# Kernel optimization log

Hardware: AMD Instinct MI355X
Metric: run time of the kernel (lower is better)

The kernel has to match this reference:

```python
import jax, jax.numpy as jnp
import numpy as np

N, E, H, NF, MN, ME = 4096, 65536, 128, 4, 8, 4
DEPTH, RATIO, NT = 5, 0.2, 2


def _k_list():
    ks, n = [], N
    for _ in range(DEPTH):
        n = int(np.ceil(RATIO * n))
        ks.append(n)
    return ks

K_LIST = _k_list()  # [820, 164, 33, 7, 2]


def _gcn(A, x, W, b, fill):
    # GCNConv on dense adjacency: D^-1/2 (A + fill*I) D^-1/2 @ (x W) + b
    n = A.shape[0]
    Ah = A + fill * jnp.eye(n, dtype=A.dtype)
    deg = jnp.sum(Ah, axis=1)
    dinv = jnp.where(deg > 0, jax.lax.rsqrt(jnp.maximum(deg, 1e-12)), 0.0)
    return (dinv[:, None] * Ah * dinv[None, :]) @ (x @ W) + b


def _augment(A):
    # GraphUNet.augment_adj: remove self loops, add weight-1 loops, A@A, remove self loops
    n = A.shape[0]
    eye = jnp.eye(n, dtype=A.dtype)
    A1 = A * (1.0 - eye) + eye
    A2 = A1 @ A1
    return A2 * (1.0 - eye)


def _topk_pool(A, x, w, k):
    # TopKPooling: score = tanh(x.w / ||w||), keep top-k, scale kept features by score
    score = jnp.tanh((x @ w) / jnp.linalg.norm(w))
    sv, perm = jax.lax.top_k(score, k)
    return x[perm] * sv[:, None], A[perm][:, perm], perm


def _graph_unet(A0, x, Wd0, bd0, Wd, bd, pool_w, Wu, bu):
    act = jax.nn.relu
    x = act(_gcn(A0, x, Wd0, bd0, 2.0))  # improved GCN: fill=2
    xs, As, perms = [x], [A0], []
    A = A0
    for i in range(DEPTH):
        A = _augment(A)
        x, A, perm = _topk_pool(A, x, pool_w[i], K_LIST[i])
        x = act(_gcn(A, x, Wd[i], bd[i], 2.0))
        if i < DEPTH - 1:
            xs.append(x)
            As.append(A)
        perms.append(perm)
    for i in range(DEPTH):
        j = DEPTH - 1 - i
        res, Aj, perm = xs[j], As[j], perms[j]
        up = jnp.zeros_like(res).at[perm].set(x)
        x = _gcn(Aj, res + up, Wu[i], bu[i], 2.0)  # sum_res=True
        if i < DEPTH - 1:
            x = act(x)
    return x


def _forward(F_0, mesh_node, mesh_edge, Wm, bm, Wd0, bd0, Wd, bd, pool_w,
             Wu, bu, Wout, bout, edge_index, n_time):
    src, dst = edge_index[0], edge_index[1]
    A = jnp.zeros((N, N), jnp.float32).at[dst, src].add(1.0)  # dst aggregates from src
    h = jnp.zeros((N, H), jnp.float32)
    F_cur = F_0
    Fs = []
    for _ in range(n_time):
        node_attr = jnp.concatenate([F_cur, mesh_node, h], axis=1)
        # Input: per-edge cat([x_i, x_j, e]) -> Linear -> scatter-sum by dst
        msg = jnp.concatenate([node_attr[dst], node_attr[src], mesh_edge], axis=1) @ Wm + bm
        h1 = jax.nn.relu(jax.ops.segment_sum(msg, dst, num_segments=N))
        h2 = _graph_unet(A, h1, Wd0, bd0, Wd, bd, pool_w, Wu, bu)
        h = jax.lax.stop_gradient(h2)
        h2 = jax.nn.relu(h2)
        F_next = _gcn(A, jnp.concatenate([h1, h2], axis=1), Wout, bout, 1.0)
        Fs.append(F_next)
        F_cur = jax.lax.stop_gradient(F_next)
    return jnp.stack(Fs, axis=1)  # [N, n_time, NF]


def setup_inputs() -> dict:
    key = jax.random.key(0)
    ks = jax.random.split(key, 12)
    s = 0.05
    node_in = NF + MN + H
    return {
        "F_0": jax.random.normal(ks[0], (N, NF), jnp.float32),
        "mesh_node": jax.random.normal(ks[1], (N, MN), jnp.float32),
        "mesh_edge": jax.random.normal(ks[2], (E, ME), jnp.float32),
        "Wm": jax.random.normal(ks[3], (2 * node_in + ME, H), jnp.float32) * s,
        "bm": jnp.zeros((H,), jnp.float32),
        "Wd0": jax.random.normal(ks[4], (H, H), jnp.float32) * s,
        "bd0": jnp.zeros((H,), jnp.float32),
        "Wd": jax.random.normal(ks[5], (DEPTH, H, H), jnp.float32) * s,
        "bd": jnp.zeros((DEPTH, H), jnp.float32),
        "pool_w": jax.random.normal(ks[6], (DEPTH, H), jnp.float32) * s,
        "Wu": jax.random.normal(ks[7], (DEPTH, H, H), jnp.float32) * s,
        "bu": jnp.zeros((DEPTH, H), jnp.float32),
        "Wout": jax.random.normal(ks[8], (2 * H, NF), jnp.float32) * s,
        "bout": jnp.zeros((NF,), jnp.float32),
        "edge_index": jax.random.randint(ks[9], (2, E), 0, N, dtype=jnp.int32),
        "n_time": NT,
    }


def reference(F_0, mesh_node, mesh_edge, Wm, bm, Wd0, bd0, Wd, bd, pool_w,
              Wu, bu, Wout, bout, edge_index, n_time):
    return _forward(F_0, mesh_node, mesh_edge, Wm, bm, Wd0, bd0, Wd, bd,
                    pool_w, Wu, bu, Wout, bout, edge_index, n_time)
```

## Files before the change

kernel.cpp:

```cpp
#include <hip/hip_runtime.h>
#include <math.h>

#define NN 4096
#define EE 65536
#define H 128
#define NF 4
#define MNODE 8
#define MEDGE 4
#define NT 2

__global__ void k_count(const int* __restrict__ dst, int* __restrict__ cnt) {
  int e = blockIdx.x * 256 + threadIdx.x;
  if (e < EE) atomicAdd(&cnt[dst[e]], 1);
}

__global__ void k_scan(const int* __restrict__ cnt, int* __restrict__ rp) {
  __shared__ int sh[1024];
  int t = threadIdx.x;
  int v0 = cnt[4*t], v1 = cnt[4*t+1], v2 = cnt[4*t+2], v3 = cnt[4*t+3];
  int p1 = v0, p2 = v0 + v1, p3 = p2 + v2, tot = p3 + v3;
  sh[t] = tot; __syncthreads();
  for (int off = 1; off < 1024; off <<= 1) {
    int add = (t >= off) ? sh[t-off] : 0;
    __syncthreads();
    sh[t] += add;
    __syncthreads();
  }
  int base = sh[t] - tot;
  rp[4*t] = base; rp[4*t+1] = base + p1; rp[4*t+2] = base + p2; rp[4*t+3] = base + p3;
  if (t == 1023) rp[NN] = sh[t];
}

__global__ void k_fill(const int* __restrict__ ei, int* __restrict__ cursor, int* __restrict__ cols) {
  int e = blockIdx.x * 256 + threadIdx.x;
  if (e < EE) {
    int d = ei[EE + e], s = ei[e];
    int pos = atomicAdd(&cursor[d], 1);
    cols[pos] = s;
  }
}

__global__ void k_dinv0(const int* __restrict__ cnt, float* __restrict__ d2, float* __restrict__ d1) {
  int i = blockIdx.x * 256 + threadIdx.x;
  if (i < NN) {
    float c = (float)cnt[i];
    d2[i] = 1.f / sqrtf(c + 2.f);
    d1[i] = 1.f / sqrtf(c + 1.f);
  }
}

__global__ void k_pwnorm(const float* __restrict__ pw, float* __restrict__ pwn) {
  int l = blockIdx.x, t = threadIdx.x;
  float a = pw[l*H + t], b = pw[l*H + 64 + t];
  float s = a*a + b*b;
  for (int off = 32; off > 0; off >>= 1) s += __shfl_down(s, off);
  if (t == 0) pwn[l] = sqrtf(s);
}

__global__ void k_segS(const int* __restrict__ dst, const float* __restrict__ me, float* __restrict__ S) {
  int e = blockIdx.x * 256 + threadIdx.x;
  if (e < EE) {
    int d = dst[e];
#pragma unroll
    for (int m = 0; m < MEDGE; m++) atomicAdd(&S[d*MEDGE + m], me[e*MEDGE + m]);
  }
}

__device__ __forceinline__ void score_epilogue(float v, int row, int t,
                                               const float* pw, const float* pwn1,
                                               float* scoreo, unsigned long long* keyso,
                                               int* ranko, float* r2) {
  float sp = v * pw[t];
  for (int off = 32; off > 0; off >>= 1) sp += __shfl_down(sp, off);
  if ((t & 63) == 0) r2[t >> 6] = sp;
  __syncthreads();
  if (t == 0) {
    float s = r2[0] + r2[1];
    float sc = tanhf(s / pwn1[0]);
    scoreo[row] = sc;
    float s2 = sc + 0.0f;
    unsigned u = __float_as_uint(s2);
    u ^= (unsigned)(((int)u >> 31)) | 0x80000000u;
    keyso[row] = ((unsigned long long)u << 12) | (unsigned)(4095 - row);
    ranko[row] = 0;
  }
}

__global__ void k_mm_cat(const float* __restrict__ F, const float* __restrict__ mn,
                         const float* __restrict__ h, const float* __restrict__ Wm,
                         float* __restrict__ P, float* __restrict__ Q) {
  __shared__ float as[140];
  int row = blockIdx.x, t = threadIdx.x;
  for (int c = t; c < 140; c += 128) {
    float v;
    if (c < NF) v = F[row*NF + c];
    else if (c < NF + MNODE) v = mn[row*MNODE + (c - NF)];
    else v = h[(size_t)row*H + (c - NF - MNODE)];
    as[c] = v;
  }
  __syncthreads();
  const float* BQ = Wm + 140*H;
  float ap = 0.f, aq = 0.f;
  for (int kk = 0; kk < 140; kk++) {
    float a = as[kk];
    ap += a * Wm[kk*H + t];
    aq += a * BQ[kk*H + t];
  }
  P[(size_t)row*H + t] = ap;
  Q[(size_t)row*H + t] = aq;
}

__global__ void k_spmm_h1_mm(const float* __restrict__ Q, const int* __restrict__ rp,
                             const int* __restrict__ cols, const float* __restrict__ Pm,
                             const float* __restrict__ bm, const float* __restrict__ S,
                             const float* __restrict__ WmB, const int* __restrict__ cnt,
                             const float* __restrict__ Wd0, const float* __restrict__ dinv2,
                             float* __restrict__ h1, float* __restrict__ tsb) {
  __shared__ float hs[128];
  int i = blockIdx.x, t = threadIdx.x;
  float acc = 0.f;
  int beg = rp[i], end = rp[i+1];
  for (int e = beg; e < end; e++) acc += Q[(size_t)cols[e]*H + t];
  float v = (float)cnt[i] * (Pm[(size_t)i*H + t] + bm[t]) + acc;
#pragma unroll
  for (int m = 0; m < MEDGE; m++) v += S[i*MEDGE + m] * WmB[m*H + t];
  v = fmaxf(v, 0.f);
  h1[(size_t)i*H + t] = v;
  hs[t] = v;
  __syncthreads();
  float a2 = 0.f;
  for (int kk = 0; kk < H; kk++) a2 += hs[kk] * Wd0[kk*H + t];
  tsb[(size_t)i*H + t] = a2 * dinv2[i];
}

__global__ void k_spmm_fused(const float* __restrict__ ts, const int* __restrict__ rp,
                             const int* __restrict__ cols, const float* __restrict__ dinv,
                             float fill, const float* __restrict__ bias, int relu,
                             float* __restrict__ out,
                             const float* __restrict__ pw, const float* __restrict__ pwn1,
                             float* __restrict__ scoreo, unsigned long long* __restrict__ keyso,
                             int* __restrict__ ranko) {
  __shared__ float r2[2];
  int i = blockIdx.x, t = threadIdx.x;
  float acc = 0.f;
  int beg = rp[i], end = rp[i+1];
  for (int e = beg; e < end; e++) acc += ts[(size_t)cols[e]*H + t];
  float v;
  if (dinv) {
    v = dinv[i] * (acc + fill * ts[(size_t)i*H + t]) + bias[t];
    if (relu) v = fmaxf(v, 0.f);
  } else v = acc;
  out[(size_t)i*H + t] = v;
  if (pw) score_epilogue(v, i, t, pw, pwn1, scoreo, keyso, ranko, r2);
}

__global__ void k_count_rank(const unsigned long long* __restrict__ keys, int n,
                             int* __restrict__ rank) {
  __shared__ unsigned long long sk[256];
  int t = threadIdx.x;
  int j = blockIdx.y * 256 + t;
  sk[t] = (j < n) ? keys[j] : 0ull;
  __syncthreads();
  int i = blockIdx.x * 256 + t;
  if (i >= n) return;
  unsigned long long ki = keys[i];
  int r = 0;
#pragma unroll 8
  for (int jj = 0; jj < 256; jj++) r += (sk[jj] > ki) ? 1 : 0;
  if (r) atomicAdd(&rank[i], r);
}

__global__ void k_select(const float* __restrict__ score, const int* __restrict__ rank,
                         int n, int k, int* __restrict__ perm, float* __restrict__ sv,
                         int* __restrict__ inv) {
  int i = blockIdx.x * 256 + threadIdx.x;
  if (i < n) {
    int r = rank[i];
    inv[i] = r;
    if (r < k) { perm[r] = i; sv[r] = score[i]; }
  }
}

__global__ void k_mm_pool(const float* __restrict__ x, const int* __restrict__ perm,
                          const float* __restrict__ sv, const float* __restrict__ B,
                          float* __restrict__ C, const float* __restrict__ dinv) {
  __shared__ float as[128];
  int row = blockIdx.x, t = threadIdx.x;
  as[t] = x[(size_t)perm[row]*H + t] * sv[row];
  __syncthreads();
  float acc = 0.f;
  for (int kk = 0; kk < H; kk++) acc += as[kk] * B[kk*H + t];
  C[(size_t)row*H + t] = acc * dinv[row];
}

__global__ void k_mm_rb(const float* __restrict__ A, const float* __restrict__ B,
                        float* __restrict__ C, const float* __restrict__ dinv) {
  __shared__ float as[128];
  int row = blockIdx.x, t = threadIdx.x;
  as[t] = A[(size_t)row*H + t];
  __syncthreads();
  float acc = 0.f;
  for (int kk = 0; kk < H; kk++) acc += as[kk] * B[kk*H + t];
  C[(size_t)row*H + t] = acc * dinv[row];
}

__global__ void k_pool_small(const float* __restrict__ score, const unsigned long long* __restrict__ keys,
                             const float* __restrict__ x, int n, int k,
                             int* __restrict__ perm, float* __restrict__ sv,
                             int* __restrict__ inv, float* __restrict__ xp) {
  __shared__ unsigned long long ks[256];
  __shared__ int permS[40];
  __shared__ float svS[40];
  int t = threadIdx.x;
  ks[t] = (t < n) ? keys[t] : 0ull;
  __syncthreads();
  if (t < n) {
    unsigned long long ki = ks[t];
    int r = 0;
    for (int j = 0; j < n; j++) r += (ks[j] > ki) ? 1 : 0;
    inv[t] = r;
    if (r < k) {
      float sc = score[t];
      permS[r] = t; svS[r] = sc;
      perm[r] = t; sv[r] = sc;
    }
  }
  __syncthreads();
  for (int idx = t; idx < k*H; idx += 256) {
    int r = idx >> 7, c = idx & 127;
    xp[idx] = x[(size_t)permS[r]*H + c] * svS[r];
  }
}

__global__ void k_a820_f(const int* __restrict__ rp, const int* __restrict__ cols,
                         const int* __restrict__ perm, float* __restrict__ A820,
                         float* __restrict__ dv) {
  __shared__ float acc[NN];
  __shared__ float red[256];
  int r = blockIdx.x, t = threadIdx.x;
  for (int i = t; i < NN; i += 256) acc[i] = 0.f;
  __syncthreads();
  int pi = perm[r];
  int beg = rp[pi], end = rp[pi+1];
  for (int e = beg + t; e < end; e += 256) { int c = cols[e]; if (c != pi) atomicAdd(&acc[c], 1.f); }
  if (t == 0) atomicAdd(&acc[pi], 1.f);
  for (int e0 = beg; e0 < end; e0++) {
    int c = cols[e0];
    if (c == pi) continue;
    int b2 = rp[c], e2 = rp[c+1];
    for (int e = b2 + t; e < e2; e += 256) { int c2 = cols[e]; if (c2 != c) atomicAdd(&acc[c2], 1.f); }
    if (t == 0) atomicAdd(&acc[c], 1.f);
  }
  __syncthreads();
  float local = 0.f;
  for (int cc = t; cc < 820; cc += 256) {
    float val = (cc == r) ? 0.f : acc[perm[cc]];
    A820[(size_t)r*820 + cc] = val;
    local += val;
  }
  red[t] = local; __syncthreads();
  for (int off = 128; off > 0; off >>= 1) { if (t < off) red[t] += red[t+off]; __syncthreads(); }
  if (t == 0) dv[r] = 1.f / sqrtf(red[0] + 2.f);
}

__global__ void k_gathercols(const float* __restrict__ A, int n, const int* __restrict__ perm,
                             int knext, float* __restrict__ AP) {
  int idx = blockIdx.x * 256 + threadIdx.x;
  int total = n * knext;
  if (idx >= total) return;
  int kk = idx / knext, c = idx - kk * knext;
  AP[idx] = A[(size_t)kk * n + perm[c]];
}

__global__ void k_augpool2_f(const float* __restrict__ A, const float* __restrict__ AP,
                             int n, const int* __restrict__ perm, int knext,
                             float* __restrict__ out, float* __restrict__ dv) {
  __shared__ float rowb[832];
  __shared__ float red[256];
  int r = blockIdx.x, t = threadIdx.x;
  int pr = perm[r];
  for (int i = t; i < n; i += 256) rowb[i] = A[(size_t)pr*n + i];
  __syncthreads();
  float local = 0.f;
  for (int c = t; c < knext; c += 256) {
    float dot = 0.f;
#pragma unroll 8
    for (int kk = 0; kk < n; kk++) dot += rowb[kk] * AP[(size_t)kk*knext + c];
    float val = (c == r) ? 0.f : (dot + 2.f * AP[(size_t)pr*knext + c]);
    out[(size_t)r*knext + c] = val;
    local += val;
  }
  red[t] = local; __syncthreads();
  for (int off = 128; off > 0; off >>= 1) { if (t < off) red[t] += red[t+off]; __syncthreads(); }
  if (t == 0) dv[r] = 1.f / sqrtf(red[0] + 2.f);
}

__global__ void k_augpool_small(const float* __restrict__ A, int n, const int* __restrict__ perm,
                                int knext, float* __restrict__ out, float* __restrict__ dv) {
  __shared__ float rowb[256];
  __shared__ float rsum;
  int r = blockIdx.x, t = threadIdx.x;
  int pr = perm[r];
  if (t < n) rowb[t] = A[(size_t)pr*n + t];
  if (t == 0) rsum = 0.f;
  __syncthreads();
  int g = t >> 3, lane = t & 7;
  for (int c = g; c < knext; c += 32) {
    int pc = perm[c];
    float part = 0.f;
    for (int kk = lane; kk < n; kk += 8) part += rowb[kk] * A[(size_t)kk*n + pc];
    part += __shfl_down(part, 4, 8);
    part += __shfl_down(part, 2, 8);
    part += __shfl_down(part, 1, 8);
    if (lane == 0) {
      float val = (c == r) ? 0.f : (part + 2.f * rowb[pc]);
      out[(size_t)r*knext + c] = val;
      atomicAdd(&rsum, val);
    }
  }
  __syncthreads();
  if (t == 0) dv[r] = 1.f / sqrtf(rsum + 2.f);
}

__global__ void k_dense_gcn(const float* __restrict__ A, int n, const float* __restrict__ ts,
                            const float* __restrict__ dinv, float fill, const float* __restrict__ bias,
                            int relu, float* __restrict__ out,
                            const float* __restrict__ pw, const float* __restrict__ pwn1,
                            float* __restrict__ scoreo, unsigned long long* __restrict__ keyso,
                            int* __restrict__ ranko) {
  __shared__ float r2[2];
  int i = blockIdx.x, t = threadIdx.x;
  const float* Ar = A + (size_t)i * n;
  float acc = 0.f;
  int kk = 0;
  int n4 = n & ~3;
#pragma unroll 2
  for (; kk < n4; kk += 4) {
    float a0 = Ar[kk+0], a1 = Ar[kk+1], a2 = Ar[kk+2], a3 = Ar[kk+3];
    float t0 = ts[(size_t)(kk+0)*H + t];
    float t1 = ts[(size_t)(kk+1)*H + t];
    float t2 = ts[(size_t)(kk+2)*H + t];
    float t3 = ts[(size_t)(kk+3)*H + t];
    acc += a0*t0; acc += a1*t1; acc += a2*t2; acc += a3*t3;
  }
  for (; kk < n; kk++) acc += Ar[kk] * ts[(size_t)kk*H + t];
  float v = dinv[i] * (acc + fill * ts[(size_t)i*H + t]) + bias[t];
  if (relu) v = fmaxf(v, 0.f);
  out[(size_t)i*H + t] = v;
  if (pw) score_epilogue(v, i, t, pw, pwn1, scoreo, keyso, ranko, r2);
}

__global__ void k_upproj(const float* __restrict__ xs, const int* __restrict__ inv,
                         const float* __restrict__ xcur, int kk,
                         const float* __restrict__ W, const float* __restrict__ dinv,
                         float* __restrict__ tsb) {
  __shared__ float hs[128];
  int i = blockIdx.x, t = threadIdx.x;
  int r = inv[i];
  float v = xs[(size_t)i*H + t];
  if (r < kk) v += xcur[(size_t)r*H + t];
  hs[t] = v;
  __syncthreads();
  float acc = 0.f;
  for (int k2 = 0; k2 < H; k2++) acc += hs[k2] * W[k2*H + t];
  tsb[(size_t)i*H + t] = acc * dinv[i];
}

__global__ void k_outproj_r(const float* __restrict__ h1, const float* __restrict__ hbuf,
                            const float* __restrict__ Wout, const float* __restrict__ dinv1,
                            float* __restrict__ ts2) {
  int row = blockIdx.x, t = threadIdx.x;
  float p0 = 0.f, p1 = 0.f, p2 = 0.f, p3 = 0.f;
#pragma unroll
  for (int half = 0; half < 2; half++) {
    float a = h1[(size_t)row*H + half*64 + t];
    const float* w = Wout + (half*64 + t)*4;
    p0 += a*w[0]; p1 += a*w[1]; p2 += a*w[2]; p3 += a*w[3];
    float b = fmaxf(hbuf[(size_t)row*H + half*64 + t], 0.f);
    const float* w2 = Wout + (128 + half*64 + t)*4;
    p0 += b*w2[0]; p1 += b*w2[1]; p2 += b*w2[2]; p3 += b*w2[3];
  }
  for (int off = 32; off > 0; off >>= 1) {
    p0 += __shfl_down(p0, off); p1 += __shfl_down(p1, off);
    p2 += __shfl_down(p2, off); p3 += __shfl_down(p3, off);
  }
  if (t == 0) {
    float d = dinv1[row];
    ts2[row*4+0] = d*p0; ts2[row*4+1] = d*p1; ts2[row*4+2] = d*p2; ts2[row*4+3] = d*p3;
  }
}

__global__ void k_gcn_out(const float* __restrict__ ts2, const int* __restrict__ rp,
                          const int* __restrict__ cols, const float* __restrict__ dinv1,
                          const float* __restrict__ bout, float* __restrict__ Fcur,
                          float* __restrict__ dout, int tstep) {
  int i = blockIdx.x, t = threadIdx.x;
  int f = t & 3;
  float acc = 0.f;
  int beg = rp[i], end = rp[i+1];
  for (int e = beg + (t >> 2); e < end; e += 16) acc += ts2[cols[e]*4 + f];
  for (int off = 32; off >= 4; off >>= 1) acc += __shfl_down(acc, off);
  if (t < 4) {
    float v = dinv1[i] * (acc + ts2[i*4 + f]) + bout[f];
    Fcur[i*4 + f] = v;
    dout[i*(NT*NF) + tstep*NF + f] = v;
  }
}

extern "C" void kernel_launch(void* const* d_in, const int* in_sizes, int n_in,
                              void* d_out, int out_size, void* d_ws, size_t ws_size,
                              hipStream_t stream) {
  const float* F0        = (const float*)d_in[0];
  const float* mesh_node = (const float*)d_in[1];
  const float* mesh_edge = (const float*)d_in[2];
  const float* Wm        = (const float*)d_in[3];
  const float* bm        = (const float*)d_in[4];
  const float* Wd0       = (const float*)d_in[5];
  const float* bd0       = (const float*)d_in[6];
  const float* Wd        = (const float*)d_in[7];
  const float* bd        = (const float*)d_in[8];
  const float* pool_w    = (const float*)d_in[9];
  const float* Wu        = (const float*)d_in[10];
  const float* bu        = (const float*)d_in[11];
  const float* Wout      = (const float*)d_in[12];
  const float* bout      = (const float*)d_in[13];
  const int*   ei        = (const int*)d_in[14];
  float* out = (float*)d_out;

  char* p = (char*)d_ws;
  auto carve = [&](size_t bytes) -> char* {
    char* r = p;
    p += (bytes + 255) & ~(size_t)255;
    return r;
  };
  int*   cnt    = (int*)carve((size_t)NN*4);
  int*   rp     = (int*)carve((size_t)(NN+1)*4);
  int*   cursor = (int*)carve((size_t)NN*4);
  int*   cols   = (int*)carve((size_t)EE*4);
  int*   permb  = (int*)carve((size_t)5*832*4);
  float* svb    = (float*)carve((size_t)5*832*4);
  float* dinv2  = (float*)carve((size_t)NN*4);
  float* dinv1  = (float*)carve((size_t)NN*4);
  float* pwn    = (float*)carve(8*4);
  float* S      = (float*)carve((size_t)NN*MEDGE*4);
  int*   invb   = (int*)carve((size_t)5*NN*4);
  float* P      = (float*)carve((size_t)NN*H*4);
  float* Q      = (float*)carve((size_t)NN*H*4);
  float* h1     = (float*)carve((size_t)NN*H*4);
  float* hbuf   = (float*)carve((size_t)NN*H*4);
  float* tsb    = (float*)carve((size_t)NN*H*4);
  float* tmp    = (float*)carve((size_t)NN*H*4);
  float* x0     = (float*)carve((size_t)NN*H*4);
  float* x1     = (float*)carve((size_t)820*H*4);
  float* x2     = (float*)carve((size_t)164*H*4);
  float* x3     = (float*)carve((size_t)33*H*4);
  float* x4     = (float*)carve((size_t)7*H*4);
  float* xp     = (float*)carve((size_t)820*H*4);
  float* xcur   = (float*)carve((size_t)820*H*4);
  float* score  = (float*)carve((size_t)NN*4);
  unsigned long long* keysb = (unsigned long long*)carve((size_t)NN*8);
  int*   rankb  = (int*)carve((size_t)NN*4);
  float* A820   = (float*)carve((size_t)820*820*4);
  float* A164   = (float*)carve((size_t)164*164*4);
  float* A33    = (float*)carve((size_t)33*33*4);
  float* A7     = (float*)carve((size_t)7*7*4);
  float* A2b    = (float*)carve((size_t)2*2*4);
  float* dv820  = (float*)carve(820*4);
  float* dv164  = (float*)carve(164*4);
  float* dv33   = (float*)carve(33*4);
  float* dv7    = (float*)carve(7*4);
  float* dv2    = (float*)carve(2*4);
  float* ts2    = (float*)carve((size_t)NN*NF*4);
  float* Fcur   = (float*)carve((size_t)NN*NF*4);

  float* AP = tmp;

  int* perml[5]; float* svl[5]; int* invl[5];
  for (int l = 0; l < 5; l++) {
    perml[l] = permb + l*832; svl[l] = svb + l*832; invl[l] = invb + l*NN;
  }

  hipMemsetAsync(cnt, 0, (size_t)NN*4, stream);
  hipMemsetAsync(S, 0, (size_t)NN*MEDGE*4, stream);
  hipMemsetAsync(hbuf, 0, (size_t)NN*H*4, stream);
  k_count<<<EE/256, 256, 0, stream>>>(ei + EE, cnt);
  k_scan<<<1, 1024, 0, stream>>>(cnt, rp);
  hipMemcpyAsync(cursor, rp, (size_t)NN*4, hipMemcpyDeviceToDevice, stream);
  k_fill<<<EE/256, 256, 0, stream>>>(ei, cursor, cols);
  k_dinv0<<<NN/256, 256, 0, stream>>>(cnt, dinv2, dinv1);
  k_pwnorm<<<5, 64, 0, stream>>>(pool_w, pwn);
  k_segS<<<EE/256, 256, 0, stream>>>(ei + EE, mesh_edge, S);
  hipMemcpyAsync(Fcur, F0, (size_t)NN*NF*4, hipMemcpyDeviceToDevice, stream);

  for (int step = 0; step < NT; step++) {
    k_mm_cat<<<NN, 128, 0, stream>>>(Fcur, mesh_node, hbuf, Wm, P, Q);
    k_spmm_h1_mm<<<NN, 128, 0, stream>>>(Q, rp, cols, P, bm, S, Wm + 280*H, cnt,
                                         Wd0, dinv2, h1, tsb);
    k_spmm_fused<<<NN, 128, 0, stream>>>(tsb, rp, cols, dinv2, 2.f, bd0, 1, x0,
                                         pool_w, pwn, score, keysb, rankb);

    k_count_rank<<<dim3(16, 16), 256, 0, stream>>>(keysb, NN, rankb);
    k_select<<<16, 256, 0, stream>>>(score, rankb, NN, 820, perml[0], svl[0], invl[0]);
    k_a820_f<<<820, 256, 0, stream>>>(rp, cols, perml[0], A820, dv820);
    k_mm_pool<<<820, 128, 0, stream>>>(x0, perml[0], svl[0], Wd, tsb, dv820);
    k_dense_gcn<<<820, 128, 0, stream>>>(A820, 820, tsb, dv820, 2.f, bd, 1, x1,
                                         pool_w + H, pwn + 1, score, keysb, rankb);

    k_count_rank<<<dim3(4, 4), 256, 0, stream>>>(keysb, 820, rankb);
    k_select<<<4, 256, 0, stream>>>(score, rankb, 820, 164, perml[1], svl[1], invl[1]);
    k_gathercols<<<(820*164 + 255)/256, 256, 0, stream>>>(A820, 820, perml[1], 164, AP);
    k_augpool2_f<<<164, 256, 0, stream>>>(A820, AP, 820, perml[1], 164, A164, dv164);
    k_mm_pool<<<164, 128, 0, stream>>>(x1, perml[1], svl[1], Wd + 1*H*H, tsb, dv164);
    k_dense_gcn<<<164, 128, 0, stream>>>(A164, 164, tsb, dv164, 2.f, bd + 1*H, 1, x2,
                                         pool_w + 2*H, pwn + 2, score, keysb, rankb);

    k_pool_small<<<1, 256, 0, stream>>>(score, keysb, x2, 164, 33, perml[2], svl[2], invl[2], xp);
    k_augpool_small<<<33, 256, 0, stream>>>(A164, 164, perml[2], 33, A33, dv33);
    k_mm_rb<<<33, 128, 0, stream>>>(xp, Wd + 2*H*H, tsb, dv33);
    k_dense_gcn<<<33, 128, 0, stream>>>(A33, 33, tsb, dv33, 2.f, bd + 2*H, 1, x3,
                                        pool_w + 3*H, pwn + 3, score, keysb, rankb);

    k_pool_small<<<1, 256, 0, stream>>>(score, keysb, x3, 33, 7, perml[3], svl[3], invl[3], xp);
    k_augpool_small<<<7, 256, 0, stream>>>(A33, 33, perml[3], 7, A7, dv7);
    k_mm_rb<<<7, 128, 0, stream>>>(xp, Wd + 3*H*H, tsb, dv7);
    k_dense_gcn<<<7, 128, 0, stream>>>(A7, 7, tsb, dv7, 2.f, bd + 3*H, 1, x4,
                                       pool_w + 4*H, pwn + 4, score, keysb, rankb);

    k_pool_small<<<1, 256, 0, stream>>>(score, keysb, x4, 7, 2, perml[4], svl[4], invl[4], xp);
    k_augpool_small<<<2, 256, 0, stream>>>(A7, 7, perml[4], 2, A2b, dv2);
    k_mm_rb<<<2, 128, 0, stream>>>(xp, Wd + 4*H*H, tsb, dv2);
    k_dense_gcn<<<2, 128, 0, stream>>>(A2b, 2, tsb, dv2, 2.f, bd + 4*H, 1, xcur,
                                       nullptr, nullptr, nullptr, nullptr, nullptr);

    k_upproj<<<7, 128, 0, stream>>>(x4, invl[4], xcur, 2, Wu, dv7, tsb);
    k_dense_gcn<<<7, 128, 0, stream>>>(A7, 7, tsb, dv7, 2.f, bu, 1, xcur,
                                       nullptr, nullptr, nullptr, nullptr, nullptr);
    k_upproj<<<33, 128, 0, stream>>>(x3, invl[3], xcur, 7, Wu + 1*H*H, dv33, tsb);
    k_dense_gcn<<<33, 128, 0, stream>>>(A33, 33, tsb, dv33, 2.f, bu + 1*H, 1, xcur,
                                        nullptr, nullptr, nullptr, nullptr, nullptr);
    k_upproj<<<164, 128, 0, stream>>>(x2, invl[2], xcur, 33, Wu + 2*H*H, dv164, tsb);
    k_dense_gcn<<<164, 128, 0, stream>>>(A164, 164, tsb, dv164, 2.f, bu + 2*H, 1, xcur,
                                         nullptr, nullptr, nullptr, nullptr, nullptr);
    k_upproj<<<820, 128, 0, stream>>>(x1, invl[1], xcur, 164, Wu + 3*H*H, dv820, tsb);
    k_dense_gcn<<<820, 128, 0, stream>>>(A820, 820, tsb, dv820, 2.f, bu + 3*H, 1, xcur,
                                         nullptr, nullptr, nullptr, nullptr, nullptr);
    k_upproj<<<NN, 128, 0, stream>>>(x0, invl[0], xcur, 820, Wu + 4*H*H, dinv2, tsb);
    k_spmm_fused<<<NN, 128, 0, stream>>>(tsb, rp, cols, dinv2, 2.f, bu + 4*H, 0, hbuf,
                                         nullptr, nullptr, nullptr, nullptr, nullptr);

    k_outproj_r<<<NN, 64, 0, stream>>>(h1, hbuf, Wout, dinv1, ts2);
    k_gcn_out<<<NN, 64, 0, stream>>>(ts2, rp, cols, dinv1, bout, Fcur, out, step);
  }
}
```

Baseline: 756.3 us.

## Process multiple rows per block in matmul/GCN kernels and fuse 820-node ranking

Row-per-block matmul and dense GCN kernels now handle 2 or 4 rows per block. Each weight or feature load is reused across those rows, and dense adjacency rows are staged in shared memory. The 820-node top-k rank and select pair becomes a single 1024-thread block that ranks against keys held in shared memory. The two-hop augmentation loop in the pool kernel now gives each wavefront its own neighbour instead of having the whole block walk them serially. In exchange there are fewer blocks, so occupancy and parallelism drop, and the single-block rank is serial over n per thread.

```diff
diff --git a/kernel.cpp b/kernel.cpp
--- a/kernel.cpp
+++ b/kernel.cpp
@@ -66,16 +66,20 @@
   }
 }
 
-__device__ __forceinline__ void score_epilogue(float v, int row, int t,
-                                               const float* pw, const float* pwn1,
-                                               float* scoreo, unsigned long long* keyso,
-                                               int* ranko, float* r2) {
-  float sp = v * pw[t];
-  for (int off = 32; off > 0; off >>= 1) sp += __shfl_down(sp, off);
-  if ((t & 63) == 0) r2[t >> 6] = sp;
-  __syncthreads();
-  if (t == 0) {
-    float s = r2[0] + r2[1];
+__device__ __forceinline__ void score_epilogue2(const float* vr, int i0, int n, int t,
+                                                const float* pw, const float* pwn1,
+                                                float* scoreo, unsigned long long* keyso,
+                                                int* ranko, float (*r2)[2]) {
+#pragma unroll
+  for (int r = 0; r < 2; r++) {
+    float sp = vr[r] * pw[t];
+    for (int off = 32; off > 0; off >>= 1) sp += __shfl_down(sp, off);
+    if ((t & 63) == 0) r2[r][t >> 6] = sp;
+  }
+  __syncthreads();
+  if (t < 2 && i0 + t < n) {
+    int row = i0 + t;
+    float s = r2[t][0] + r2[t][1];
     float sc = tanhf(s / pwn1[0]);
     scoreo[row] = sc;
     float s2 = sc + 0.0f;
@@ -86,51 +90,67 @@
   }
 }
 
-__global__ void k_mm_cat(const float* __restrict__ F, const float* __restrict__ mn,
-                         const float* __restrict__ h, const float* __restrict__ Wm,
-                         float* __restrict__ P, float* __restrict__ Q) {
-  __shared__ float as[140];
-  int row = blockIdx.x, t = threadIdx.x;
-  for (int c = t; c < 140; c += 128) {
-    float v;
-    if (c < NF) v = F[row*NF + c];
-    else if (c < NF + MNODE) v = mn[row*MNODE + (c - NF)];
-    else v = h[(size_t)row*H + (c - NF - MNODE)];
-    as[c] = v;
+__global__ void k_mm_cat4(const float* __restrict__ F, const float* __restrict__ mn,
+                          const float* __restrict__ h, const float* __restrict__ Wm,
+                          float* __restrict__ P, float* __restrict__ Q) {
+  __shared__ float as[4][140];
+  int i0 = blockIdx.x * 4, t = threadIdx.x;
+#pragma unroll
+  for (int r = 0; r < 4; r++) {
+    int row = i0 + r;
+    for (int c = t; c < 140; c += 128) {
+      float v;
+      if (c < NF) v = F[row*NF + c];
+      else if (c < NF + MNODE) v = mn[row*MNODE + (c - NF)];
+      else v = h[(size_t)row*H + (c - NF - MNODE)];
+      as[r][c] = v;
+    }
   }
   __syncthreads();
   const float* BQ = Wm + 140*H;
-  float ap = 0.f, aq = 0.f;
+  float p0=0,p1=0,p2=0,p3=0,q0=0,q1=0,q2=0,q3=0;
   for (int kk = 0; kk < 140; kk++) {
-    float a = as[kk];
-    ap += a * Wm[kk*H + t];
-    aq += a * BQ[kk*H + t];
-  }
-  P[(size_t)row*H + t] = ap;
-  Q[(size_t)row*H + t] = aq;
-}
-
-__global__ void k_spmm_h1_mm(const float* __restrict__ Q, const int* __restrict__ rp,
-                             const int* __restrict__ cols, const float* __restrict__ Pm,
-                             const float* __restrict__ bm, const float* __restrict__ S,
-                             const float* __restrict__ WmB, const int* __restrict__ cnt,
-                             const float* __restrict__ Wd0, const float* __restrict__ dinv2,
-                             float* __restrict__ h1, float* __restrict__ tsb) {
-  __shared__ float hs[128];
-  int i = blockIdx.x, t = threadIdx.x;
-  float acc = 0.f;
-  int beg = rp[i], end = rp[i+1];
-  for (int e = beg; e < end; e++) acc += Q[(size_t)cols[e]*H + t];
-  float v = (float)cnt[i] * (Pm[(size_t)i*H + t] + bm[t]) + acc;
-#pragma unroll
-  for (int m = 0; m < MEDGE; m++) v += S[i*MEDGE + m] * WmB[m*H + t];
-  v = fmaxf(v, 0.f);
-  h1[(size_t)i*H + t] = v;
-  hs[t] = v;
-  __syncthreads();
-  float a2 = 0.f;
-  for (int kk = 0; kk < H; kk++) a2 += hs[kk] * Wd0[kk*H + t];
-  tsb[(size_t)i*H + t] = a2 * dinv2[i];
+    float wP = Wm[kk*H + t], wQ = BQ[kk*H + t];
+    p0 += as[0][kk]*wP; p1 += as[1][kk]*wP; p2 += as[2][kk]*wP; p3 += as[3][kk]*wP;
+    q0 += as[0][kk]*wQ; q1 += as[1][kk]*wQ; q2 += as[2][kk]*wQ; q3 += as[3][kk]*wQ;
+  }
+  P[(size_t)(i0+0)*H + t] = p0; P[(size_t)(i0+1)*H + t] = p1;
+  P[(size_t)(i0+2)*H + t] = p2; P[(size_t)(i0+3)*H + t] = p3;
+  Q[(size_t)(i0+0)*H + t] = q0; Q[(size_t)(i0+1)*H + t] = q1;
+  Q[(size_t)(i0+2)*H + t] = q2; Q[(size_t)(i0+3)*H + t] = q3;
+}
+
+__global__ void k_spmm_h1_mm4(const float* __restrict__ Q, const int* __restrict__ rp,
+                              const int* __restrict__ cols, const float* __restrict__ Pm,
+                              const float* __restrict__ bm, const float* __restrict__ S,
+                              const float* __restrict__ WmB, const int* __restrict__ cnt,
+                              const float* __restrict__ Wd0, const float* __restrict__ dinv2,
+                              float* __restrict__ h1, float* __restrict__ tsb) {
+  __shared__ float hs[4][128];
+  int i0 = blockIdx.x * 4, t = threadIdx.x;
+#pragma unroll
+  for (int r = 0; r < 4; r++) {
+    int i = i0 + r;
+    float acc = 0.f;
+    int beg = rp[i], end = rp[i+1];
+    for (int e = beg; e < end; e++) acc += Q[(size_t)cols[e]*H + t];
+    float v = (float)cnt[i] * (Pm[(size_t)i*H + t] + bm[t]) + acc;
+#pragma unroll
+    for (int m = 0; m < MEDGE; m++) v += S[i*MEDGE + m] * WmB[m*H + t];
+    v = fmaxf(v, 0.f);
+    h1[(size_t)i*H + t] = v;
+    hs[r][t] = v;
+  }
+  __syncthreads();
+  float a0=0,a1=0,a2=0,a3=0;
+  for (int kk = 0; kk < H; kk++) {
+    float w = Wd0[kk*H + t];
+    a0 += hs[0][kk]*w; a1 += hs[1][kk]*w; a2 += hs[2][kk]*w; a3 += hs[3][kk]*w;
+  }
+  tsb[(size_t)(i0+0)*H + t] = a0 * dinv2[i0+0];
+  tsb[(size_t)(i0+1)*H + t] = a1 * dinv2[i0+1];
+  tsb[(size_t)(i0+2)*H + t] = a2 * dinv2[i0+2];
+  tsb[(size_t)(i0+3)*H + t] = a3 * dinv2[i0+3];
 }
 
 __global__ void k_spmm_fused(const float* __restrict__ ts, const int* __restrict__ rp,
@@ -140,7 +160,7 @@
                              const float* __restrict__ pw, const float* __restrict__ pwn1,
                              float* __restrict__ scoreo, unsigned long long* __restrict__ keyso,
                              int* __restrict__ ranko) {
-  __shared__ float r2[2];
+  __shared__ float r2s[2];
   int i = blockIdx.x, t = threadIdx.x;
   float acc = 0.f;
   int beg = rp[i], end = rp[i+1];
@@ -151,7 +171,22 @@
     if (relu) v = fmaxf(v, 0.f);
   } else v = acc;
   out[(size_t)i*H + t] = v;
-  if (pw) score_epilogue(v, i, t, pw, pwn1, scoreo, keyso, ranko, r2);
+  if (pw) {
+    float sp = v * pw[t];
+    for (int off = 32; off > 0; off >>= 1) sp += __shfl_down(sp, off);
+    if ((t & 63) == 0) r2s[t >> 6] = sp;
+    __syncthreads();
+    if (t == 0) {
+      float s = r2s[0] + r2s[1];
+      float sc = tanhf(s / pwn1[0]);
+      scoreo[i] = sc;
+      float s2 = sc + 0.0f;
+      unsigned u = __float_as_uint(s2);
+      u ^= (unsigned)(((int)u >> 31)) | 0x80000000u;
+      keyso[i] = ((unsigned long long)u << 12) | (unsigned)(4095 - i);
+      ranko[i] = 0;
+    }
+  }
 }
 
 __global__ void k_count_rank(const unsigned long long* __restrict__ keys, int n,
@@ -181,16 +216,39 @@
   }
 }
 
-__global__ void k_mm_pool(const float* __restrict__ x, const int* __restrict__ perm,
-                          const float* __restrict__ sv, const float* __restrict__ B,
-                          float* __restrict__ C, const float* __restrict__ dinv) {
-  __shared__ float as[128];
-  int row = blockIdx.x, t = threadIdx.x;
-  as[t] = x[(size_t)perm[row]*H + t] * sv[row];
-  __syncthreads();
-  float acc = 0.f;
-  for (int kk = 0; kk < H; kk++) acc += as[kk] * B[kk*H + t];
-  C[(size_t)row*H + t] = acc * dinv[row];
+__global__ void k_rank820(const float* __restrict__ score, const unsigned long long* __restrict__ keys,
+                          int n, int k, int* __restrict__ perm, float* __restrict__ sv,
+                          int* __restrict__ inv) {
+  __shared__ unsigned long long ks[832];
+  int t = threadIdx.x;
+  for (int i = t; i < n; i += 1024) ks[i] = keys[i];
+  __syncthreads();
+  if (t < n) {
+    unsigned long long ki = ks[t];
+    int r = 0;
+    for (int j = 0; j < n; j++) r += (ks[j] > ki) ? 1 : 0;
+    inv[t] = r;
+    if (r < k) { perm[r] = t; sv[r] = score[t]; }
+  }
+}
+
+__global__ void k_mm_pool2(const float* __restrict__ x, const int* __restrict__ perm,
+                           const float* __restrict__ sv, const float* __restrict__ B,
+                           float* __restrict__ C, const float* __restrict__ dinv, int n) {
+  __shared__ float as[2][128];
+  int i0 = blockIdx.x * 2, t = threadIdx.x;
+  int nr = n - i0; if (nr > 2) nr = 2;
+#pragma unroll
+  for (int r = 0; r < 2; r++) if (r < nr)
+    as[r][t] = x[(size_t)perm[i0+r]*H + t] * sv[i0+r];
+  __syncthreads();
+  float a0 = 0.f, a1 = 0.f;
+  for (int kk = 0; kk < H; kk++) {
+    float w = B[kk*H + t];
+    a0 += as[0][kk]*w; a1 += as[1][kk]*w;
+  }
+  if (0 < nr) C[(size_t)(i0+0)*H + t] = a0 * dinv[i0+0];
+  if (1 < nr) C[(size_t)(i0+1)*H + t] = a1 * dinv[i0+1];
 }
 
 __global__ void k_mm_rb(const float* __restrict__ A, const float* __restrict__ B,
@@ -244,12 +302,13 @@
   int beg = rp[pi], end = rp[pi+1];
   for (int e = beg + t; e < end; e += 256) { int c = cols[e]; if (c != pi) atomicAdd(&acc[c], 1.f); }
   if (t == 0) atomicAdd(&acc[pi], 1.f);
-  for (int e0 = beg; e0 < end; e0++) {
+  int wv = t >> 6, ln = t & 63;
+  for (int e0 = beg + wv; e0 < end; e0 += 4) {
     int c = cols[e0];
     if (c == pi) continue;
     int b2 = rp[c], e2 = rp[c+1];
-    for (int e = b2 + t; e < e2; e += 256) { int c2 = cols[e]; if (c2 != c) atomicAdd(&acc[c2], 1.f); }
-    if (t == 0) atomicAdd(&acc[c], 1.f);
+    for (int e = b2 + ln; e < e2; e += 64) { int c2 = cols[e]; if (c2 != c) atomicAdd(&acc[c2], 1.f); }
+    if (ln == 0) atomicAdd(&acc[c], 1.f);
   }
   __syncthreads();
   float local = 0.f;
@@ -322,48 +381,71 @@
   if (t == 0) dv[r] = 1.f / sqrtf(rsum + 2.f);
 }
 
-__global__ void k_dense_gcn(const float* __restrict__ A, int n, const float* __restrict__ ts,
-                            const float* __restrict__ dinv, float fill, const float* __restrict__ bias,
-                            int relu, float* __restrict__ out,
-                            const float* __restrict__ pw, const float* __restrict__ pwn1,
-                            float* __restrict__ scoreo, unsigned long long* __restrict__ keyso,
-                            int* __restrict__ ranko) {
-  __shared__ float r2[2];
-  int i = blockIdx.x, t = threadIdx.x;
-  const float* Ar = A + (size_t)i * n;
-  float acc = 0.f;
+__global__ void k_dense_gcn2(const float* __restrict__ A, int n, const float* __restrict__ ts,
+                             const float* __restrict__ dinv, float fill, const float* __restrict__ bias,
+                             int relu, float* __restrict__ out,
+                             const float* __restrict__ pw, const float* __restrict__ pwn1,
+                             float* __restrict__ scoreo, unsigned long long* __restrict__ keyso,
+                             int* __restrict__ ranko) {
+  __shared__ float As[2*832];
+  __shared__ float r2[2][2];
+  int i0 = blockIdx.x * 2, t = threadIdx.x;
+  int nr = n - i0; if (nr > 2) nr = 2;
+#pragma unroll
+  for (int r = 0; r < 2; r++) if (r < nr)
+    for (int kk = t; kk < n; kk += 128)
+      As[r*832 + kk] = A[(size_t)(i0+r)*n + kk];
+  __syncthreads();
+  float a0 = 0.f, a1 = 0.f;
   int kk = 0;
-  int n4 = n & ~3;
+  int n2 = n & ~1;
 #pragma unroll 2
-  for (; kk < n4; kk += 4) {
-    float a0 = Ar[kk+0], a1 = Ar[kk+1], a2 = Ar[kk+2], a3 = Ar[kk+3];
+  for (; kk < n2; kk += 2) {
     float t0 = ts[(size_t)(kk+0)*H + t];
     float t1 = ts[(size_t)(kk+1)*H + t];
-    float t2 = ts[(size_t)(kk+2)*H + t];
-    float t3 = ts[(size_t)(kk+3)*H + t];
-    acc += a0*t0; acc += a1*t1; acc += a2*t2; acc += a3*t3;
-  }
-  for (; kk < n; kk++) acc += Ar[kk] * ts[(size_t)kk*H + t];
-  float v = dinv[i] * (acc + fill * ts[(size_t)i*H + t]) + bias[t];
-  if (relu) v = fmaxf(v, 0.f);
-  out[(size_t)i*H + t] = v;
-  if (pw) score_epilogue(v, i, t, pw, pwn1, scoreo, keyso, ranko, r2);
-}
-
-__global__ void k_upproj(const float* __restrict__ xs, const int* __restrict__ inv,
-                         const float* __restrict__ xcur, int kk,
-                         const float* __restrict__ W, const float* __restrict__ dinv,
-                         float* __restrict__ tsb) {
-  __shared__ float hs[128];
-  int i = blockIdx.x, t = threadIdx.x;
-  int r = inv[i];
-  float v = xs[(size_t)i*H + t];
-  if (r < kk) v += xcur[(size_t)r*H + t];
-  hs[t] = v;
-  __syncthreads();
-  float acc = 0.f;
-  for (int k2 = 0; k2 < H; k2++) acc += hs[k2] * W[k2*H + t];
-  tsb[(size_t)i*H + t] = acc * dinv[i];
+    a0 += As[kk]*t0;       a0 += As[kk+1]*t1;
+    a1 += As[832+kk]*t0;   a1 += As[832+kk+1]*t1;
+  }
+  for (; kk < n; kk++) {
+    float tv = ts[(size_t)kk*H + t];
+    a0 += As[kk]*tv; a1 += As[832+kk]*tv;
+  }
+  float vr[2] = {0.f, 0.f};
+  float aa[2] = {a0, a1};
+#pragma unroll
+  for (int r = 0; r < 2; r++) if (r < nr) {
+    int i = i0 + r;
+    float v = dinv[i] * (aa[r] + fill * ts[(size_t)i*H + t]) + bias[t];
+    if (relu) v = fmaxf(v, 0.f);
+    out[(size_t)i*H + t] = v;
+    vr[r] = v;
+  }
+  if (pw) score_epilogue2(vr, i0, n, t, pw, pwn1, scoreo, keyso, ranko, r2);
+}
+
+__global__ void k_upproj2(const float* __restrict__ xs, const int* __restrict__ inv,
+                          const float* __restrict__ xcur, int kk_,
+                          const float* __restrict__ W, const float* __restrict__ dinv,
+                          int n, float* __restrict__ tsb) {
+  __shared__ float hs[2][128];
+  int i0 = blockIdx.x * 2, t = threadIdx.x;
+  int nr = n - i0; if (nr > 2) nr = 2;
+#pragma unroll
+  for (int r = 0; r < 2; r++) if (r < nr) {
+    int i = i0 + r;
+    int rr = inv[i];
+    float v = xs[(size_t)i*H + t];
+    if (rr < kk_) v += xcur[(size_t)rr*H + t];
+    hs[r][t] = v;
+  }
+  __syncthreads();
+  float a0 = 0.f, a1 = 0.f;
+  for (int k2 = 0; k2 < H; k2++) {
+    float w = W[k2*H + t];
+    a0 += hs[0][k2]*w; a1 += hs[1][k2]*w;
+  }
+  if (0 < nr) tsb[(size_t)(i0+0)*H + t] = a0 * dinv[i0+0];
+  if (1 < nr) tsb[(size_t)(i0+1)*H + t] = a1 * dinv[i0+1];
 }
 
 __global__ void k_outproj_r(const float* __restrict__ h1, const float* __restrict__ hbuf,
@@ -493,58 +575,57 @@
   hipMemcpyAsync(Fcur, F0, (size_t)NN*NF*4, hipMemcpyDeviceToDevice, stream);
 
   for (int step = 0; step < NT; step++) {
-    k_mm_cat<<<NN, 128, 0, stream>>>(Fcur, mesh_node, hbuf, Wm, P, Q);
-    k_spmm_h1_mm<<<NN, 128, 0, stream>>>(Q, rp, cols, P, bm, S, Wm + 280*H, cnt,
-                                         Wd0, dinv2, h1, tsb);
+    k_mm_cat4<<<NN/4, 128, 0, stream>>>(Fcur, mesh_node, hbuf, Wm, P, Q);
+    k_spmm_h1_mm4<<<NN/4, 128, 0, stream>>>(Q, rp, cols, P, bm, S, Wm + 280*H, cnt,
+                                            Wd0, dinv2, h1, tsb);
     k_spmm_fused<<<NN, 128, 0, stream>>>(tsb, rp, cols, dinv2, 2.f, bd0, 1, x0,
                                          pool_w, pwn, score, keysb, rankb);
 
     k_count_rank<<<dim3(16, 16), 256, 0, stream>>>(keysb, NN, rankb);
     k_select<<<16, 256, 0, stream>>>(score, rankb, NN, 820, perml[0], svl[0], invl[0]);
     k_a820_f<<<820, 256, 0, stream>>>(rp, cols, perml[0], A820, dv820);
-    k_mm_pool<<<820, 128, 0, stream>>>(x0, perml[0], svl[0], Wd, tsb, dv820);
-    k_dense_gcn<<<820, 128, 0, stream>>>(A820, 820, tsb, dv820, 2.f, bd, 1, x1,
-                                         pool_w + H, pwn + 1, score, keysb, rankb);
-
-    k_count_rank<<<dim3(4, 4), 256, 0, stream>>>(keysb, 820, rankb);
-    k_select<<<4, 256, 0, stream>>>(score, rankb, 820, 164, perml[1], svl[1], invl[1]);
+    k_mm_pool2<<<410, 128, 0, stream>>>(x0, perml[0], svl[0], Wd, tsb, dv820, 820);
+    k_dense_gcn2<<<410, 128, 0, stream>>>(A820, 820, tsb, dv820, 2.f, bd, 1, x1,
+                                          pool_w + H, pwn + 1, score, keysb, rankb);
+
+    k_rank820<<<1, 1024, 0, stream>>>(score, keysb, 820, 164, perml[1], svl[1], invl[1]);
     k_gathercols<<<(820*164 + 255)/256, 256, 0, stream>>>(A820, 820, perml[1], 164, AP);
     k_augpool2_f<<<164, 256, 0, stream>>>(A820, AP, 820, perml[1], 164, A164, dv164);
-    k_mm_pool<<<164, 128, 0, stream>>>(x1, perml[1], svl[1], Wd + 1*H*H, tsb, dv164);
-    k_dense_gcn<<<164, 128, 0, stream>>>(A164, 164, tsb, dv164, 2.f, bd + 1*H, 1, x2,
+    k_mm_pool2<<<82, 128, 0, stream>>>(x1, perml[1], svl[1], Wd + 1*H*H, tsb, dv164, 164);
+    k_dense_gcn2<<<82, 128, 0, stream>>>(A164, 164, tsb, dv164, 2.f, bd + 1*H, 1, x2,
                                          pool_w + 2*H, pwn + 2, score, keysb, rankb);
 
     k_pool_small<<<1, 256, 0, stream>>>(score, keysb, x2, 164, 33, perml[2], svl[2], invl[2], xp);
     k_augpool_small<<<33, 256, 0, stream>>>(A164, 164, perml[2], 33, A33, dv33);
     k_mm_rb<<<33, 128, 0, stream>>>(xp, Wd + 2*H*H, tsb, dv33);
-    k_dense_gcn<<<33, 128, 0, stream>>>(A33, 33, tsb, dv33, 2.f, bd + 2*H, 1, x3,
-                                        pool_w + 3*H, pwn + 3, score, keysb, rankb);
+    k_dense_gcn2<<<17, 128, 0, stream>>>(A33, 33, tsb, dv33, 2.f, bd + 2*H, 1, x3,
+                                         pool_w + 3*H, pwn + 3, score, keysb, rankb);
 
     k_pool_small<<<1, 256, 0, stream>>>(score, keysb, x3, 33, 7, perml[3], svl[3], invl[3], xp);
     k_augpool_small<<<7, 256, 0, stream>>>(A33, 33, perml[3], 7, A7, dv7);
     k_mm_rb<<<7, 128, 0, stream>>>(xp, Wd + 3*H*H, tsb, dv7);
-    k_dense_gcn<<<7, 128, 0, stream>>>(A7, 7, tsb, dv7, 2.f, bd + 3*H, 1, x4,
-                                       pool_w + 4*H, pwn + 4, score, keysb, rankb);
+    k_dense_gcn2<<<4, 128, 0, stream>>>(A7, 7, tsb, dv7, 2.f, bd + 3*H, 1, x4,
+                                        pool_w + 4*H, pwn + 4, score, keysb, rankb);
 
     k_pool_small<<<1, 256, 0, stream>>>(score, keysb, x4, 7, 2, perml[4], svl[4], invl[4], xp);
     k_augpool_small<<<2, 256, 0, stream>>>(A7, 7, perml[4], 2, A2b, dv2);
     k_mm_rb<<<2, 128, 0, stream>>>(xp, Wd + 4*H*H, tsb, dv2);
-    k_dense_gcn<<<2, 128, 0, stream>>>(A2b, 2, tsb, dv2, 2.f, bd + 4*H, 1, xcur,
-                                       nullptr, nullptr, nullptr, nullptr, nullptr);
-
-    k_upproj<<<7, 128, 0, stream>>>(x4, invl[4], xcur, 2, Wu, dv7, tsb);
-    k_dense_gcn<<<7, 128, 0, stream>>>(A7, 7, tsb, dv7, 2.f, bu, 1, xcur,
-                                       nullptr, nullptr, nullptr, nullptr, nullptr);
-    k_upproj<<<33, 128, 0, stream>>>(x3, invl[3], xcur, 7, Wu + 1*H*H, dv33, tsb);
-    k_dense_gcn<<<33, 128, 0, stream>>>(A33, 33, tsb, dv33, 2.f, bu + 1*H, 1, xcur,
+    k_dense_gcn2<<<1, 128, 0, stream>>>(A2b, 2, tsb, dv2, 2.f, bd + 4*H, 1, xcur,
                                         nullptr, nullptr, nullptr, nullptr, nullptr);
-    k_upproj<<<164, 128, 0, stream>>>(x2, invl[2], xcur, 33, Wu + 2*H*H, dv164, tsb);
-    k_dense_gcn<<<164, 128, 0, stream>>>(A164, 164, tsb, dv164, 2.f, bu + 2*H, 1, xcur,
+
+    k_upproj2<<<4, 128, 0, stream>>>(x4, invl[4], xcur, 2, Wu, dv7, 7, tsb);
+    k_dense_gcn2<<<4, 128, 0, stream>>>(A7, 7, tsb, dv7, 2.f, bu, 1, xcur,
+                                        nullptr, nullptr, nullptr, nullptr, nullptr);
+    k_upproj2<<<17, 128, 0, stream>>>(x3, invl[3], xcur, 7, Wu + 1*H*H, dv33, 33, tsb);
+    k_dense_gcn2<<<17, 128, 0, stream>>>(A33, 33, tsb, dv33, 2.f, bu + 1*H, 1, xcur,
                                          nullptr, nullptr, nullptr, nullptr, nullptr);
-    k_upproj<<<820, 128, 0, stream>>>(x1, invl[1], xcur, 164, Wu + 3*H*H, dv820, tsb);
-    k_dense_gcn<<<820, 128, 0, stream>>>(A820, 820, tsb, dv820, 2.f, bu + 3*H, 1, xcur,
+    k_upproj2<<<82, 128, 0, stream>>>(x2, invl[2], xcur, 33, Wu + 2*H*H, dv164, 164, tsb);
+    k_dense_gcn2<<<82, 128, 0, stream>>>(A164, 164, tsb, dv164, 2.f, bu + 2*H, 1, xcur,
                                          nullptr, nullptr, nullptr, nullptr, nullptr);
-    k_upproj<<<NN, 128, 0, stream>>>(x0, invl[0], xcur, 820, Wu + 4*H*H, dinv2, tsb);
+    k_upproj2<<<410, 128, 0, stream>>>(x1, invl[1], xcur, 164, Wu + 3*H*H, dv820, 820, tsb);
+    k_dense_gcn2<<<410, 128, 0, stream>>>(A820, 820, tsb, dv820, 2.f, bu + 3*H, 1, xcur,
+                                          nullptr, nullptr, nullptr, nullptr, nullptr);
+    k_upproj2<<<NN/2, 128, 0, stream>>>(x0, invl[0], xcur, 820, Wu + 4*H*H, dinv2, NN, tsb);
     k_spmm_fused<<<NN, 128, 0, stream>>>(tsb, rp, cols, dinv2, 2.f, bu + 4*H, 0, hbuf,
                                          nullptr, nullptr, nullptr, nullptr, nullptr);
 
```

Result: slower. 934.7 us (+23.6%).
